# Performance work log

Measured on AMD Instinct MI355X. Metric: run time of the kernel, lower is better.

The kernel has to match this reference:

```python
import jax, jax.numpy as jnp
import numpy as np

B, T, F = 4096, 256, 20
VOCAB, EMB = 1281, 4
UNITS = (64, 32, 32, 32)


def setup_inputs() -> dict:
    key = jax.random.key(0)
    ks = jax.random.split(key, 16)
    feats = jax.random.normal(ks[0], (B, T, F), jnp.float32)
    ids = jax.random.randint(ks[1], (B, T), 0, VOCAB).astype(jnp.float32)
    input_tensor = feats.at[:, :, 1].set(ids)  # column 1 = org ids
    W_emb = jax.random.normal(ks[2], (VOCAB, EMB), jnp.float32) * 0.1
    in_dims = (F - 2 + 1 + EMB,) + UNITS[:-1]  # (23, 64, 32, 32)
    out = {"input_tensor": input_tensor, "W_emb": W_emb}
    for i, (din, u) in enumerate(zip(in_dims, UNITS)):
        out[f"k{i}"] = jax.random.normal(ks[3 + 3 * i], (din, 3 * u), jnp.float32) * 0.1
        out[f"rk{i}"] = jax.random.normal(ks[4 + 3 * i], (u, 3 * u), jnp.float32) * 0.1
        out[f"b{i}"] = jnp.zeros((2, 3 * u), jnp.float32)  # [input_bias, recurrent_bias] (reset_after)
    out["Wd"] = jax.random.normal(ks[15], (UNITS[-1], 2), jnp.float32) * 0.1
    out["bd"] = jnp.zeros((2,), jnp.float32)
    return out


def _gru(h, x, k, rk, b):
    # Keras GRUCell, reset_after=True (TF2 default)
    mx = x @ k + b[0]
    mh = h @ rk + b[1]
    xz, xr, xh = jnp.split(mx, 3, axis=-1)
    hz, hr, hh = jnp.split(mh, 3, axis=-1)
    z = jax.nn.sigmoid(xz + hz)
    r = jax.nn.sigmoid(xr + hr)
    hc = jnp.tanh(xh + r * hh)
    return z * h + (1.0 - z) * hc


def reference(input_tensor, W_emb, k0, rk0, b0, k1, rk1, b1, k2, rk2, b2, k3, rk3, b3, Wd, bd):
    f0 = input_tensor[:, :, :1]                      # [B,T,1]
    ids = input_tensor[:, :, 1].astype(jnp.int32)    # [B,T]
    rest = input_tensor[:, :, 2:]                    # [B,T,F-2]
    emb = W_emb[ids]                                 # [B,T,EMB]
    x = jnp.concatenate([f0, rest, emb], axis=-1)    # [B,T,F+3]
    xs = jnp.swapaxes(x, 0, 1)                       # [T,B,F+3]
    bsz = x.shape[0]
    h_init = tuple(jnp.zeros((bsz, u), x.dtype) for u in UNITS)
    layer_params = ((k0, rk0, b0), (k1, rk1, b1), (k2, rk2, b2), (k3, rk3, b3))

    def step(carry, xt):
        hs = []
        inp = xt
        for h, (k, rk, b) in zip(carry, layer_params):
            h = _gru(h, inp, k, rk, b)
            hs.append(h)
            inp = h
        return tuple(hs), None

    hs, _ = jax.lax.scan(step, h_init, xs)
    # return_sequences + [:, -1, :] == final hidden state of last layer
    logits = hs[-1] @ Wd + bd
    return jax.nn.softmax(logits, axis=-1)
```

## Files before the change

### kernel.cpp

```cpp
#include <hip/hip_runtime.h>


typedef __attribute__((ext_vector_type(8))) __bf16 bf16x8;
typedef __attribute__((ext_vector_type(4))) float f32x4;

#define TT 256
#define FF 20
#define BT 16
#define CH 64
#define SH0 72
#define SH1 40
#define XSTR 648
#define NTHR 768

__device__ __forceinline__ f32x4 mfma16(bf16x8 a, bf16x8 b, f32x4 c) {
  return __builtin_amdgcn_mfma_f32_16x16x32_bf16(a, b, c, 0, 0, 0);
}

__device__ __forceinline__ float sigm(float x) {
  return __builtin_amdgcn_rcpf(1.f + __builtin_amdgcn_exp2f(-1.44269504f * x));
}
__device__ __forceinline__ float tanh_(float x) {
  return __builtin_amdgcn_rcpf(1.f + __builtin_amdgcn_exp2f(-2.88539008f * x)) * 2.f - 1.f;
}

__device__ __forceinline__ bf16x8 bfragW(const float* W, int Kreal, int N,
                                         int ncol, int kbase) {
  bf16x8 r;
#pragma unroll
  for (int j = 0; j < 8; ++j) {
    int k = kbase + j;
    r[j] = (__bf16)(k < Kreal ? W[k * N + ncol] : 0.f);
  }
  return r;
}

extern "C" __global__ void __launch_bounds__(NTHR, 3)
gru4(const float* __restrict__ inp, const float* __restrict__ Wemb,
     const float* __restrict__ k0, const float* __restrict__ rk0, const float* __restrict__ b0,
     const float* __restrict__ k1, const float* __restrict__ rk1, const float* __restrict__ b1,
     const float* __restrict__ k2, const float* __restrict__ rk2, const float* __restrict__ b2,
     const float* __restrict__ k3, const float* __restrict__ rk3, const float* __restrict__ b3,
     const float* __restrict__ Wd, const float* __restrict__ bd,
     float* __restrict__ out)
{
  __shared__ __align__(16) __bf16 x_ch[CH * XSTR];
  __shared__ __align__(16) __bf16 h0_lds[2][BT * SH0];
  __shared__ __align__(16) __bf16 h1_lds[2][BT * SH1];
  __shared__ __align__(16) __bf16 h2_lds[2][BT * SH1];
  __shared__ __align__(16) __bf16 h3_lds[2][BT * SH1];
  __shared__ __align__(16) float h3f[BT * 32];

  const int tid  = threadIdx.x;
  const int lane = tid & 63;
  const int w    = tid >> 6;
  const int col  = lane & 15;
  const int kb   = (lane >> 4) * 8;
  const int rowq = (lane >> 4) * 4;
  const long bbase = (long)blockIdx.x * BT;
  const float* binp = inp + bbase * TT * FF;

  bf16x8 zf;
#pragma unroll
  for (int j = 0; j < 8; ++j) zf[j] = (__bf16)0.f;

  bf16x8 Wz0 = zf, Wz1 = zf, Wz2 = zf;
  bf16x8 Wr0 = zf, Wr1 = zf, Wr2 = zf;
  bf16x8 Wgx0 = zf, Wgx1 = zf, Wgx2 = zf;
  bf16x8 Wgh0 = zf, Wgh1 = zf, Wgh2 = zf;
  float bz = 0.f, br = 0.f, bxh = 0.f, bhh = 0.f;
  const __bf16 *A0b = x_ch, *A1b = x_ch, *A2b = x_ch;
  int D0 = 0, D1 = 0, D2 = 0;
  __bf16* Wwr0 = (__bf16*)h3f;
  int WD = 0, wstride = SH1;
  int lay = 0;
  bool doLo = false, doHi = false, threeA = false;

  if (w < 6) {
    lay = 0; threeA = true;
    const int sl = (w < 4) ? (w >> 1) : (w - 2);
    doLo = (w >= 4) || ((w & 1) == 0);
    doHi = (w >= 4) || ((w & 1) == 1);
    const int u = sl * 16 + col;
    Wz0 = bfragW(k0, 23, 192, u, kb);
    Wz1 = bfragW(rk0, 64, 192, u, kb);
    Wz2 = bfragW(rk0, 64, 192, u, 32 + kb);
    Wr0 = bfragW(k0, 23, 192, 64 + u, kb);
    Wr1 = bfragW(rk0, 64, 192, 64 + u, kb);
    Wr2 = bfragW(rk0, 64, 192, 64 + u, 32 + kb);
    Wgx0 = bfragW(k0, 23, 192, 128 + u, kb);
    Wgh1 = bfragW(rk0, 64, 192, 128 + u, kb);
    Wgh2 = bfragW(rk0, 64, 192, 128 + u, 32 + kb);
    bz  = b0[u] + b0[192 + u];
    br  = b0[64 + u] + b0[192 + 64 + u];
    bxh = b0[128 + u];
    bhh = b0[192 + 128 + u];
    A1b = &h0_lds[0][col * SH0 + kb];      D1 = BT * SH0;
    A2b = &h0_lds[0][col * SH0 + 32 + kb]; D2 = BT * SH0;
    Wwr0 = &h0_lds[0][rowq * SH0 + sl * 16 + col];
    WD = BT * SH0; wstride = SH0;
  } else if (w < 8) {
    lay = 1; threeA = true; doLo = doHi = true;
    const int u = (w - 6) * 16 + col;
    Wz0 = bfragW(k1, 64, 96, u, kb);
    Wz1 = bfragW(k1, 64, 96, u, 32 + kb);
    Wz2 = bfragW(rk1, 32, 96, u, kb);
    Wr0 = bfragW(k1, 64, 96, 32 + u, kb);
    Wr1 = bfragW(k1, 64, 96, 32 + u, 32 + kb);
    Wr2 = bfragW(rk1, 32, 96, 32 + u, kb);
    Wgx0 = bfragW(k1, 64, 96, 64 + u, kb);
    Wgx1 = bfragW(k1, 64, 96, 64 + u, 32 + kb);
    Wgh2 = bfragW(rk1, 32, 96, 64 + u, kb);
    bz  = b1[u] + b1[96 + u];
    br  = b1[32 + u] + b1[96 + 32 + u];
    bxh = b1[64 + u];
    bhh = b1[96 + 64 + u];
    A0b = &h0_lds[0][col * SH0 + kb];      D0 = BT * SH0;
    A1b = &h0_lds[0][col * SH0 + 32 + kb]; D1 = BT * SH0;
    A2b = &h1_lds[0][col * SH1 + kb];      D2 = BT * SH1;
    Wwr0 = &h1_lds[0][rowq * SH1 + (w - 6) * 16 + col];
    WD = BT * SH1; wstride = SH1;
  } else if (w < 10) {
    lay = 2; threeA = false; doLo = doHi = true;
    const int u = (w - 8) * 16 + col;
    Wz0 = bfragW(k2, 32, 96, u, kb);
    Wz1 = bfragW(rk2, 32, 96, u, kb);
    Wr0 = bfragW(k2, 32, 96, 32 + u, kb);
    Wr1 = bfragW(rk2, 32, 96, 32 + u, kb);
    Wgx0 = bfragW(k2, 32, 96, 64 + u, kb);
    Wgh1 = bfragW(rk2, 32, 96, 64 + u, kb);
    bz  = b2[u] + b2[96 + u];
    br  = b2[32 + u] + b2[96 + 32 + u];
    bxh = b2[64 + u];
    bhh = b2[96 + 64 + u];
    A0b = &h1_lds[0][col * SH1 + kb]; D0 = BT * SH1;
    A1b = &h2_lds[0][col * SH1 + kb]; D1 = BT * SH1;
    A2b = A1b; D2 = D1;
    Wwr0 = &h2_lds[0][rowq * SH1 + (w - 8) * 16 + col];
    WD = BT * SH1; wstride = SH1;
  } else {
    lay = 3; threeA = false; doLo = doHi = true;
    const int u = (w - 10) * 16 + col;
    Wz0 = bfragW(k3, 32, 96, u, kb);
    Wz1 = bfragW(rk3, 32, 96, u, kb);
    Wr0 = bfragW(k3, 32, 96, 32 + u, kb);
    Wr1 = bfragW(rk3, 32, 96, 32 + u, kb);
    Wgx0 = bfragW(k3, 32, 96, 64 + u, kb);
    Wgh1 = bfragW(rk3, 32, 96, 64 + u, kb);
    bz  = b3[u] + b3[96 + u];
    br  = b3[32 + u] + b3[96 + 32 + u];
    bxh = b3[64 + u];
    bhh = b3[96 + 64 + u];
    A0b = &h2_lds[0][col * SH1 + kb]; D0 = BT * SH1;
    A1b = &h3_lds[0][col * SH1 + kb]; D1 = BT * SH1;
    A2b = A1b; D2 = D1;
    Wwr0 = &h3_lds[0][rowq * SH1 + (w - 10) * 16 + col];
    WD = BT * SH1; wstride = SH1;
  }

  const __bf16* xb = &x_ch[col * 40 + kb];

  {
    __bf16* p0 = (__bf16*)h0_lds;
    for (int i = tid; i < 2 * BT * SH0; i += NTHR) p0[i] = (__bf16)0.f;
    __bf16* p1 = (__bf16*)h1_lds;
    __bf16* p2 = (__bf16*)h2_lds;
    __bf16* p3 = (__bf16*)h3_lds;
    for (int i = tid; i < 2 * BT * SH1; i += NTHR) {
      p1[i] = (__bf16)0.f; p2[i] = (__bf16)0.f; p3[i] = (__bf16)0.f;
    }
  }
  float hreg[4] = {0.f, 0.f, 0.f, 0.f};
  __syncthreads();

  for (int s = 0; s < TT + 3; ++s) {
    if ((s & (CH - 1)) == 0 && s < TT) {
      for (int idx = tid; idx < BT * CH; idx += NTHR) {
        const int row = idx >> 6;
        const int tg  = idx & (CH - 1);
        const float* p = binp + ((long)row * TT + s + tg) * FF;
        float4 v0 = *(const float4*)(p);
        float4 v1 = *(const float4*)(p + 4);
        float4 v2 = *(const float4*)(p + 8);
        float4 v3 = *(const float4*)(p + 12);
        float4 v4 = *(const float4*)(p + 16);
        float4 e  = *(const float4*)(Wemb + 4 * (int)v0.y);
        __bf16* d = &x_ch[tg * XSTR + row * 40];
        bf16x8 q0 = {(__bf16)v0.x, (__bf16)v0.z, (__bf16)v0.w, (__bf16)v1.x,
                     (__bf16)v1.y, (__bf16)v1.z, (__bf16)v1.w, (__bf16)v2.x};
        bf16x8 q1 = {(__bf16)v2.y, (__bf16)v2.z, (__bf16)v2.w, (__bf16)v3.x,
                     (__bf16)v3.y, (__bf16)v3.z, (__bf16)v3.w, (__bf16)v4.x};
        bf16x8 q2 = {(__bf16)v4.y, (__bf16)v4.z, (__bf16)v4.w, (__bf16)e.x,
                     (__bf16)e.y,  (__bf16)e.z,  (__bf16)e.w,  (__bf16)0.f};
        *(bf16x8*)(d)      = q0;
        *(bf16x8*)(d + 8)  = q1;
        *(bf16x8*)(d + 16) = q2;
        *(bf16x8*)(d + 24) = zf;
      }
      __syncthreads();
    }

    const int pb = (s + 1) & 1;
    const int qb = s & 1;
    const int t  = s - lay;

    if (t >= 0 && t < TT) {
      const __bf16* a0p = (lay == 0) ? (xb + (s & (CH - 1)) * XSTR)
                                     : (A0b + pb * D0);
      bf16x8 A0 = *(const bf16x8*)a0p;
      bf16x8 A1 = *(const bf16x8*)(A1b + pb * D1);
      f32x4 az  = {bz, bz, bz, bz};
      f32x4 ar  = {br, br, br, br};
      f32x4 axh = {bxh, bxh, bxh, bxh};
      f32x4 ahh = {bhh, bhh, bhh, bhh};
      az  = mfma16(A0, Wz0, az);   az  = mfma16(A1, Wz1, az);
      ar  = mfma16(A0, Wr0, ar);   ar  = mfma16(A1, Wr1, ar);
      axh = mfma16(A0, Wgx0, axh); axh = mfma16(A1, Wgx1, axh);
      ahh = mfma16(A0, Wgh0, ahh); ahh = mfma16(A1, Wgh1, ahh);
      if (threeA) {
        bf16x8 A2 = *(const bf16x8*)(A2b + pb * D2);
        az  = mfma16(A2, Wz2, az);
        ar  = mfma16(A2, Wr2, ar);
        axh = mfma16(A2, Wgx2, axh);
        ahh = mfma16(A2, Wgh2, ahh);
      }
      __bf16* wr = Wwr0 + qb * WD;

#define GATE(r) { \
        float z  = sigm(az[r]); \
        float rg = sigm(ar[r]); \
        float hc = tanh_(fmaf(rg, ahh[r], axh[r])); \
        float hn = fmaf(z, hreg[r] - hc, hc); \
        hreg[r] = hn; \
        wr[(r) * wstride] = (__bf16)hn; }

      if (doLo) { GATE(0); GATE(1); }
      if (doHi) { GATE(2); GATE(3); }
#undef GATE
    }

    __syncthreads();
  }

  if (w >= 10) {
#pragma unroll
    for (int r = 0; r < 4; ++r)
      h3f[(rowq + r) * 32 + (w - 10) * 16 + col] = hreg[r];
  }
  __syncthreads();

  if (tid < BT) {
    float l0 = bd[0], l1 = bd[1];
#pragma unroll
    for (int u = 0; u < 32; ++u) {
      float h = h3f[tid * 32 + u];
      l0 = fmaf(h, Wd[2 * u], l0);
      l1 = fmaf(h, Wd[2 * u + 1], l1);
    }
    float m = fmaxf(l0, l1);
    float e0 = __builtin_amdgcn_exp2f((l0 - m) * 1.44269504f);
    float e1 = __builtin_amdgcn_exp2f((l1 - m) * 1.44269504f);
    float inv = 1.f / (e0 + e1);
    out[(bbase + tid) * 2 + 0] = e0 * inv;
    out[(bbase + tid) * 2 + 1] = e1 * inv;
  }
}

extern "C" void kernel_launch(void* const* d_in, const int* in_sizes, int n_in,
                              void* d_out, int out_size, void* d_ws, size_t ws_size,
                              hipStream_t stream) {
  const float* inp  = (const float*)d_in[0];
  const float* Wemb = (const float*)d_in[1];
  const float* k0   = (const float*)d_in[2];
  const float* rk0  = (const float*)d_in[3];
  const float* b0   = (const float*)d_in[4];
  const float* k1   = (const float*)d_in[5];
  const float* rk1  = (const float*)d_in[6];
  const float* b1   = (const float*)d_in[7];
  const float* k2   = (const float*)d_in[8];
  const float* rk2  = (const float*)d_in[9];
  const float* b2   = (const float*)d_in[10];
  const float* k3   = (const float*)d_in[11];
  const float* rk3  = (const float*)d_in[12];
  const float* b3   = (const float*)d_in[13];
  const float* Wd   = (const float*)d_in[14];
  const float* bd   = (const float*)d_in[15];
  float* out = (float*)d_out;

  const int Btot = in_sizes[0] / (TT * FF);
  dim3 grid(Btot / BT);
  gru4<<<grid, NTHR, 0, stream>>>(inp, Wemb, k0, rk0, b0, k1, rk1, b1,
                                  k2, rk2, b2, k3, rk3, b3, Wd, bd, out);
}
```

Baseline: 345.5 us.

## Software-pipeline GRU steps so gate math precedes barrier and MFMAs follow

```diff
diff --git a/kernel.cpp b/kernel.cpp
--- a/kernel.cpp
+++ b/kernel.cpp
@@ -173,74 +173,82 @@
   float hreg[4] = {0.f, 0.f, 0.f, 0.f};
   __syncthreads();
 
-  for (int s = 0; s < TT + 3; ++s) {
-    if ((s & (CH - 1)) == 0 && s < TT) {
-      for (int idx = tid; idx < BT * CH; idx += NTHR) {
-        const int row = idx >> 6;
-        const int tg  = idx & (CH - 1);
-        const float* p = binp + ((long)row * TT + s + tg) * FF;
-        float4 v0 = *(const float4*)(p);
-        float4 v1 = *(const float4*)(p + 4);
-        float4 v2 = *(const float4*)(p + 8);
-        float4 v3 = *(const float4*)(p + 12);
-        float4 v4 = *(const float4*)(p + 16);
-        float4 e  = *(const float4*)(Wemb + 4 * (int)v0.y);
-        __bf16* d = &x_ch[tg * XSTR + row * 40];
-        bf16x8 q0 = {(__bf16)v0.x, (__bf16)v0.z, (__bf16)v0.w, (__bf16)v1.x,
-                     (__bf16)v1.y, (__bf16)v1.z, (__bf16)v1.w, (__bf16)v2.x};
-        bf16x8 q1 = {(__bf16)v2.y, (__bf16)v2.z, (__bf16)v2.w, (__bf16)v3.x,
-                     (__bf16)v3.y, (__bf16)v3.z, (__bf16)v3.w, (__bf16)v4.x};
-        bf16x8 q2 = {(__bf16)v4.y, (__bf16)v4.z, (__bf16)v4.w, (__bf16)e.x,
-                     (__bf16)e.y,  (__bf16)e.z,  (__bf16)e.w,  (__bf16)0.f};
-        *(bf16x8*)(d)      = q0;
-        *(bf16x8*)(d + 8)  = q1;
-        *(bf16x8*)(d + 16) = q2;
-        *(bf16x8*)(d + 24) = zf;
-      }
-      __syncthreads();
+  auto stageX = [&](int s) {
+    for (int idx = tid; idx < BT * CH; idx += NTHR) {
+      const int row = idx >> 6;
+      const int tq  = idx & (CH - 1);
+      const float* p = binp + ((long)row * TT + s + tq) * FF;
+      float4 v0 = *(const float4*)(p);
+      float4 v1 = *(const float4*)(p + 4);
+      float4 v2 = *(const float4*)(p + 8);
+      float4 v3 = *(const float4*)(p + 12);
+      float4 v4 = *(const float4*)(p + 16);
+      float4 e  = *(const float4*)(Wemb + 4 * (int)v0.y);
+      __bf16* d = &x_ch[tq * XSTR + row * 40];
+      bf16x8 q0 = {(__bf16)v0.x, (__bf16)v0.z, (__bf16)v0.w, (__bf16)v1.x,
+                   (__bf16)v1.y, (__bf16)v1.z, (__bf16)v1.w, (__bf16)v2.x};
+      bf16x8 q1 = {(__bf16)v2.y, (__bf16)v2.z, (__bf16)v2.w, (__bf16)v3.x,
+                   (__bf16)v3.y, (__bf16)v3.z, (__bf16)v3.w, (__bf16)v4.x};
+      bf16x8 q2 = {(__bf16)v4.y, (__bf16)v4.z, (__bf16)v4.w, (__bf16)e.x,
+                   (__bf16)e.y,  (__bf16)e.z,  (__bf16)e.w,  (__bf16)0.f};
+      *(bf16x8*)(d)      = q0;
+      *(bf16x8*)(d + 8)  = q1;
+      *(bf16x8*)(d + 16) = q2;
+      *(bf16x8*)(d + 24) = zf;
     }
-
-    const int pb = (s + 1) & 1;
-    const int qb = s & 1;
-    const int t  = s - lay;
-
-    if (t >= 0 && t < TT) {
-      const __bf16* a0p = (lay == 0) ? (xb + (s & (CH - 1)) * XSTR)
-                                     : (A0b + pb * D0);
-      bf16x8 A0 = *(const bf16x8*)a0p;
-      bf16x8 A1 = *(const bf16x8*)(A1b + pb * D1);
-      f32x4 az  = {bz, bz, bz, bz};
-      f32x4 ar  = {br, br, br, br};
-      f32x4 axh = {bxh, bxh, bxh, bxh};
-      f32x4 ahh = {bhh, bhh, bhh, bhh};
-      az  = mfma16(A0, Wz0, az);   az  = mfma16(A1, Wz1, az);
-      ar  = mfma16(A0, Wr0, ar);   ar  = mfma16(A1, Wr1, ar);
-      axh = mfma16(A0, Wgx0, axh); axh = mfma16(A1, Wgx1, axh);
-      ahh = mfma16(A0, Wgh0, ahh); ahh = mfma16(A1, Wgh1, ahh);
-      if (threeA) {
-        bf16x8 A2 = *(const bf16x8*)(A2b + pb * D2);
-        az  = mfma16(A2, Wz2, az);
-        ar  = mfma16(A2, Wr2, ar);
-        axh = mfma16(A2, Wgx2, axh);
-        ahh = mfma16(A2, Wgh2, ahh);
-      }
-      __bf16* wr = Wwr0 + qb * WD;
-
-#define GATE(r) { \
-        float z  = sigm(az[r]); \
-        float rg = sigm(ar[r]); \
-        float hc = tanh_(fmaf(rg, ahh[r], axh[r])); \
-        float hn = fmaf(z, hreg[r] - hc, hc); \
-        hreg[r] = hn; \
-        wr[(r) * wstride] = (__bf16)hn; }
-
-      if (doLo) { GATE(0); GATE(1); }
-      if (doHi) { GATE(2); GATE(3); }
+  };
+
+  f32x4 az0 = {0.f,0.f,0.f,0.f}, ar0 = az0, axh0 = az0, ahh0 = az0;
+  f32x4 az1 = az0, ar1 = az0, axh1 = az0, ahh1 = az0;
+
+#define GATE(O, r) { \
+    float z  = sigm(az##O[r]); \
+    float rg = sigm(ar##O[r]); \
+    float hc = tanh_(fmaf(rg, ahh##O[r], axh##O[r])); \
+    float hn = fmaf(z, hreg[r] - hc, hc); \
+    hreg[r] = hn; \
+    wr[(r) * wstride] = (__bf16)hn; }
+
+#define ITER(S, N, O) { \
+    const int tg_ = (S) - lay - 1; \
+    if (tg_ >= 0 && tg_ < TT) { \
+      __bf16* wr = Wwr0 + ((S) & 1) * WD; \
+      if (doLo) { GATE(O, 0) GATE(O, 1) } \
+      if (doHi) { GATE(O, 2) GATE(O, 3) } \
+    } \
+    __syncthreads(); \
+    if (((S) & (CH - 1)) == 0 && (S) < TT) { stageX(S); __syncthreads(); } \
+    const int tm_ = (S) - lay; \
+    if (tm_ >= 0 && tm_ < TT) { \
+      const int rb_ = (S) & 1; \
+      const __bf16* a0p = (lay == 0) ? (xb + ((S) & (CH - 1)) * XSTR) \
+                                     : (A0b + rb_ * D0); \
+      bf16x8 A0 = *(const bf16x8*)a0p; \
+      bf16x8 A1 = *(const bf16x8*)(A1b + rb_ * D1); \
+      az##N  = (f32x4){bz, bz, bz, bz}; \
+      ar##N  = (f32x4){br, br, br, br}; \
+      axh##N = (f32x4){bxh, bxh, bxh, bxh}; \
+      ahh##N = (f32x4){bhh, bhh, bhh, bhh}; \
+      az##N  = mfma16(A0, Wz0, az##N);   az##N  = mfma16(A1, Wz1, az##N); \
+      ar##N  = mfma16(A0, Wr0, ar##N);   ar##N  = mfma16(A1, Wr1, ar##N); \
+      axh##N = mfma16(A0, Wgx0, axh##N); axh##N = mfma16(A1, Wgx1, axh##N); \
+      ahh##N = mfma16(A0, Wgh0, ahh##N); ahh##N = mfma16(A1, Wgh1, ahh##N); \
+      if (threeA) { \
+        bf16x8 A2 = *(const bf16x8*)(A2b + rb_ * D2); \
+        az##N  = mfma16(A2, Wz2, az##N); \
+        ar##N  = mfma16(A2, Wr2, ar##N); \
+        axh##N = mfma16(A2, Wgx2, axh##N); \
+        ahh##N = mfma16(A2, Wgh2, ahh##N); \
+      } \
+    } \
+  }
+
+  for (int s2 = 0; s2 < TT + 4; s2 += 2) {
+    ITER(s2, 0, 1)
+    ITER(s2 + 1, 1, 0)
+  }
+#undef ITER
 #undef GATE
-    }
-
-    __syncthreads();
-  }
 
   if (w >= 10) {
 #pragma unroll
```

Result: no change. 347.3 us (+0.5%).

## Assign one wavefront per GRU layer and sync once per eight-step supergroup

Applied to the files above, without the earlier changes.

```diff
diff --git a/kernel.cpp b/kernel.cpp
--- a/kernel.cpp
+++ b/kernel.cpp
@@ -7,11 +7,16 @@
 #define TT 256
 #define FF 20
 #define BT 16
-#define CH 64
-#define SH0 72
-#define SH1 40
-#define XSTR 648
-#define NTHR 768
+#define KS 8
+#define NSUP 35
+#define XSTR 40
+#define H0STR 72
+#define H1STR 40
+#define XPL (16 * XSTR)
+#define H0PL (16 * H0STR)
+#define H1PL (16 * H1STR)
+#define W0PL (16 * H0STR)
+#define NTHR 256
 
 __device__ __forceinline__ f32x4 mfma16(bf16x8 a, bf16x8 b, f32x4 c) {
   return __builtin_amdgcn_mfma_f32_16x16x32_bf16(a, b, c, 0, 0, 0);
@@ -35,7 +40,7 @@
   return r;
 }
 
-extern "C" __global__ void __launch_bounds__(NTHR, 3)
+extern "C" __global__ void __launch_bounds__(NTHR, 1)
 gru4(const float* __restrict__ inp, const float* __restrict__ Wemb,
      const float* __restrict__ k0, const float* __restrict__ rk0, const float* __restrict__ b0,
      const float* __restrict__ k1, const float* __restrict__ rk1, const float* __restrict__ b1,
@@ -44,19 +49,20 @@
      const float* __restrict__ Wd, const float* __restrict__ bd,
      float* __restrict__ out)
 {
-  __shared__ __align__(16) __bf16 x_ch[CH * XSTR];
-  __shared__ __align__(16) __bf16 h0_lds[2][BT * SH0];
-  __shared__ __align__(16) __bf16 h1_lds[2][BT * SH1];
-  __shared__ __align__(16) __bf16 h2_lds[2][BT * SH1];
-  __shared__ __align__(16) __bf16 h3_lds[2][BT * SH1];
+  __shared__ __align__(16) __bf16 xring[16 * XPL];
+  __shared__ __align__(16) __bf16 h0ring[16 * H0PL];
+  __shared__ __align__(16) __bf16 h1ring[16 * H1PL];
+  __shared__ __align__(16) __bf16 h2ring[16 * H1PL];
+  __shared__ __align__(16) __bf16 h3s[2 * H1PL];
+  __shared__ __align__(16) __bf16 w0p[12 * W0PL];
   __shared__ __align__(16) float h3f[BT * 32];
 
   const int tid  = threadIdx.x;
   const int lane = tid & 63;
   const int w    = tid >> 6;
-  const int col  = lane & 15;
+  const int c    = lane & 15;
   const int kb   = (lane >> 4) * 8;
-  const int rowq = (lane >> 4) * 4;
+  const int rq   = (lane >> 4) * 4;
   const long bbase = (long)blockIdx.x * BT;
   const float* binp = inp + bbase * TT * FF;
 
@@ -64,191 +70,357 @@
 #pragma unroll
   for (int j = 0; j < 8; ++j) zf[j] = (__bf16)0.f;
 
-  bf16x8 Wz0 = zf, Wz1 = zf, Wz2 = zf;
-  bf16x8 Wr0 = zf, Wr1 = zf, Wr2 = zf;
-  bf16x8 Wgx0 = zf, Wgx1 = zf, Wgx2 = zf;
-  bf16x8 Wgh0 = zf, Wgh1 = zf, Wgh2 = zf;
-  float bz = 0.f, br = 0.f, bxh = 0.f, bhh = 0.f;
-  const __bf16 *A0b = x_ch, *A1b = x_ch, *A2b = x_ch;
-  int D0 = 0, D1 = 0, D2 = 0;
-  __bf16* Wwr0 = (__bf16*)h3f;
-  int WD = 0, wstride = SH1;
-  int lay = 0;
-  bool doLo = false, doHi = false, threeA = false;
-
-  if (w < 6) {
-    lay = 0; threeA = true;
-    const int sl = (w < 4) ? (w >> 1) : (w - 2);
-    doLo = (w >= 4) || ((w & 1) == 0);
-    doHi = (w >= 4) || ((w & 1) == 1);
-    const int u = sl * 16 + col;
-    Wz0 = bfragW(k0, 23, 192, u, kb);
-    Wz1 = bfragW(rk0, 64, 192, u, kb);
-    Wz2 = bfragW(rk0, 64, 192, u, 32 + kb);
-    Wr0 = bfragW(k0, 23, 192, 64 + u, kb);
-    Wr1 = bfragW(rk0, 64, 192, 64 + u, kb);
-    Wr2 = bfragW(rk0, 64, 192, 64 + u, 32 + kb);
-    Wgx0 = bfragW(k0, 23, 192, 128 + u, kb);
-    Wgh1 = bfragW(rk0, 64, 192, 128 + u, kb);
-    Wgh2 = bfragW(rk0, 64, 192, 128 + u, 32 + kb);
-    bz  = b0[u] + b0[192 + u];
-    br  = b0[64 + u] + b0[192 + 64 + u];
-    bxh = b0[128 + u];
-    bhh = b0[192 + 128 + u];
-    A1b = &h0_lds[0][col * SH0 + kb];      D1 = BT * SH0;
-    A2b = &h0_lds[0][col * SH0 + 32 + kb]; D2 = BT * SH0;
-    Wwr0 = &h0_lds[0][rowq * SH0 + sl * 16 + col];
-    WD = BT * SH0; wstride = SH0;
-  } else if (w < 8) {
-    lay = 1; threeA = true; doLo = doHi = true;
-    const int u = (w - 6) * 16 + col;
-    Wz0 = bfragW(k1, 64, 96, u, kb);
-    Wz1 = bfragW(k1, 64, 96, u, 32 + kb);
-    Wz2 = bfragW(rk1, 32, 96, u, kb);
-    Wr0 = bfragW(k1, 64, 96, 32 + u, kb);
-    Wr1 = bfragW(k1, 64, 96, 32 + u, 32 + kb);
-    Wr2 = bfragW(rk1, 32, 96, 32 + u, kb);
-    Wgx0 = bfragW(k1, 64, 96, 64 + u, kb);
-    Wgx1 = bfragW(k1, 64, 96, 64 + u, 32 + kb);
-    Wgh2 = bfragW(rk1, 32, 96, 64 + u, kb);
-    bz  = b1[u] + b1[96 + u];
-    br  = b1[32 + u] + b1[96 + 32 + u];
-    bxh = b1[64 + u];
-    bhh = b1[96 + 64 + u];
-    A0b = &h0_lds[0][col * SH0 + kb];      D0 = BT * SH0;
-    A1b = &h0_lds[0][col * SH0 + 32 + kb]; D1 = BT * SH0;
-    A2b = &h1_lds[0][col * SH1 + kb];      D2 = BT * SH1;
-    Wwr0 = &h1_lds[0][rowq * SH1 + (w - 6) * 16 + col];
-    WD = BT * SH1; wstride = SH1;
-  } else if (w < 10) {
-    lay = 2; threeA = false; doLo = doHi = true;
-    const int u = (w - 8) * 16 + col;
-    Wz0 = bfragW(k2, 32, 96, u, kb);
-    Wz1 = bfragW(rk2, 32, 96, u, kb);
-    Wr0 = bfragW(k2, 32, 96, 32 + u, kb);
-    Wr1 = bfragW(rk2, 32, 96, 32 + u, kb);
-    Wgx0 = bfragW(k2, 32, 96, 64 + u, kb);
-    Wgh1 = bfragW(rk2, 32, 96, 64 + u, kb);
-    bz  = b2[u] + b2[96 + u];
-    br  = b2[32 + u] + b2[96 + 32 + u];
-    bxh = b2[64 + u];
-    bhh = b2[96 + 64 + u];
-    A0b = &h1_lds[0][col * SH1 + kb]; D0 = BT * SH1;
-    A1b = &h2_lds[0][col * SH1 + kb]; D1 = BT * SH1;
-    A2b = A1b; D2 = D1;
-    Wwr0 = &h2_lds[0][rowq * SH1 + (w - 8) * 16 + col];
-    WD = BT * SH1; wstride = SH1;
+  for (int i = tid; i < 16 * H0PL; i += NTHR) h0ring[i] = (__bf16)0.f;
+  for (int i = tid; i < 16 * H1PL; i += NTHR) { h1ring[i] = (__bf16)0.f; h2ring[i] = (__bf16)0.f; }
+  for (int i = tid; i < 2 * H1PL; i += NTHR) h3s[i] = (__bf16)0.f;
+  for (int e = tid; e < 12 * 16 * 64; e += NTHR) {
+    int p = e >> 10, rem = e & 1023, cc = rem >> 6, kk = rem & 63;
+    int g = p >> 2;
+    int gb = (g == 0) ? 0 : (g == 1) ? 64 : 128;
+    w0p[p * W0PL + cc * H0STR + kk] = (__bf16)rk0[kk * 192 + gb + (p & 3) * 16 + cc];
+  }
+
+  auto stageX = [&](int tstart) {
+    int j = tid - 128;
+    if (j >= 0) {
+      int tp = j >> 4, row = j & 15;
+      int t = tstart + tp;
+      const float* p = binp + ((long)row * TT + t) * FF;
+      float4 v0 = *(const float4*)(p);
+      float4 v1 = *(const float4*)(p + 4);
+      float4 v2 = *(const float4*)(p + 8);
+      float4 v3 = *(const float4*)(p + 12);
+      float4 v4 = *(const float4*)(p + 16);
+      float4 e  = *(const float4*)(Wemb + 4 * (int)v0.y);
+      __bf16* d = &xring[(t & 15) * XPL + row * XSTR];
+      bf16x8 q0 = {(__bf16)v0.x, (__bf16)v0.z, (__bf16)v0.w, (__bf16)v1.x,
+                   (__bf16)v1.y, (__bf16)v1.z, (__bf16)v1.w, (__bf16)v2.x};
+      bf16x8 q1 = {(__bf16)v2.y, (__bf16)v2.z, (__bf16)v2.w, (__bf16)v3.x,
+                   (__bf16)v3.y, (__bf16)v3.z, (__bf16)v3.w, (__bf16)v4.x};
+      bf16x8 q2 = {(__bf16)v4.y, (__bf16)v4.z, (__bf16)v4.w, (__bf16)e.x,
+                   (__bf16)e.y,  (__bf16)e.z,  (__bf16)e.w,  (__bf16)0.f};
+      *(bf16x8*)(d)      = q0;
+      *(bf16x8*)(d + 8)  = q1;
+      *(bf16x8*)(d + 16) = q2;
+      *(bf16x8*)(d + 24) = zf;
+    }
+  };
+  stageX(0);
+  __syncthreads();
+
+  if (w == 0) {
+    bf16x8 WzX[4], WrX[4], WxX[4];
+    f32x4 bZ[4], bR[4], bXH[4], bHH[4];
+#pragma unroll
+    for (int sl = 0; sl < 4; ++sl) {
+      const int u = sl * 16 + c;
+      WzX[sl] = bfragW(k0, 23, 192, u, kb);
+      WrX[sl] = bfragW(k0, 23, 192, 64 + u, kb);
+      WxX[sl] = bfragW(k0, 23, 192, 128 + u, kb);
+      float vz = b0[u] + b0[192 + u];
+      float vr = b0[64 + u] + b0[192 + 64 + u];
+      float vx = b0[128 + u];
+      float vh = b0[192 + 128 + u];
+      bZ[sl]  = (f32x4){vz, vz, vz, vz};
+      bR[sl]  = (f32x4){vr, vr, vr, vr};
+      bXH[sl] = (f32x4){vx, vx, vx, vx};
+      bHH[sl] = (f32x4){vh, vh, vh, vh};
+    }
+    f32x4 az[4], ar[4], ax[4], ah[4];
+    float hp[4][4];
+#pragma unroll
+    for (int sl = 0; sl < 4; ++sl)
+#pragma unroll
+      for (int r = 0; r < 4; ++r) hp[sl][r] = 0.f;
+
+    auto mfmaS = [&](int t) {
+      bf16x8 Ax = *(const bf16x8*)&xring[(t & 15) * XPL + c * XSTR + kb];
+#pragma unroll
+      for (int sl = 0; sl < 4; ++sl) {
+        az[sl] = mfma16(Ax, WzX[sl], bZ[sl]);
+        ar[sl] = mfma16(Ax, WrX[sl], bR[sl]);
+        ax[sl] = mfma16(Ax, WxX[sl], bXH[sl]);
+      }
+      const __bf16* hb = &h0ring[((t - 1) & 15) * H0PL + c * H0STR];
+      bf16x8 Ah1 = *(const bf16x8*)&hb[kb];
+      bf16x8 Ah2 = *(const bf16x8*)&hb[32 + kb];
+      const __bf16* wp = &w0p[c * H0STR + kb];
+#pragma unroll
+      for (int sl = 0; sl < 4; ++sl) {
+        bf16x8 f1 = *(const bf16x8*)&wp[sl * W0PL];
+        bf16x8 f2 = *(const bf16x8*)&wp[sl * W0PL + 32];
+        az[sl] = mfma16(Ah1, f1, az[sl]);
+        az[sl] = mfma16(Ah2, f2, az[sl]);
+      }
+#pragma unroll
+      for (int sl = 0; sl < 4; ++sl) {
+        bf16x8 f1 = *(const bf16x8*)&wp[(4 + sl) * W0PL];
+        bf16x8 f2 = *(const bf16x8*)&wp[(4 + sl) * W0PL + 32];
+        ar[sl] = mfma16(Ah1, f1, ar[sl]);
+        ar[sl] = mfma16(Ah2, f2, ar[sl]);
+      }
+#pragma unroll
+      for (int sl = 0; sl < 4; ++sl) {
+        bf16x8 f1 = *(const bf16x8*)&wp[(8 + sl) * W0PL];
+        bf16x8 f2 = *(const bf16x8*)&wp[(8 + sl) * W0PL + 32];
+        ah[sl] = mfma16(Ah1, f1, bHH[sl]);
+        ah[sl] = mfma16(Ah2, f2, ah[sl]);
+      }
+    };
+    auto gateS = [&](int t) {
+      __bf16* wr = &h0ring[(t & 15) * H0PL + rq * H0STR];
+#pragma unroll
+      for (int sl = 0; sl < 4; ++sl)
+#pragma unroll
+        for (int r = 0; r < 4; ++r) {
+          float z  = sigm(az[sl][r]);
+          float rg = sigm(ar[sl][r]);
+          float hc = tanh_(fmaf(rg, ah[sl][r], ax[sl][r]));
+          float hn = fmaf(z, hp[sl][r] - hc, hc);
+          hp[sl][r] = hn;
+          wr[r * H0STR + sl * 16 + c] = (__bf16)hn;
+        }
+    };
+
+    for (int sg = 0; sg < NSUP; ++sg) {
+      const int tb = sg * KS;
+      if (tb < TT) {
+        mfmaS(tb);
+#pragma unroll 1
+        for (int k2 = 0; k2 < KS - 1; ++k2) {
+          gateS(tb + k2);
+          mfmaS(tb + k2 + 1);
+        }
+        gateS(tb + KS - 1);
+      }
+      __syncthreads();
+    }
+  } else if (w == 1) {
+    bf16x8 Wz1[2], Wz2[2], WzH[2], Wr1[2], Wr2[2], WrH[2], Wx1[2], Wx2[2], WhH[2];
+    f32x4 bZ[2], bR[2], bXH[2], bHH[2];
+#pragma unroll
+    for (int t2 = 0; t2 < 2; ++t2) {
+      const int u = t2 * 16 + c;
+      Wz1[t2] = bfragW(k1, 64, 96, u, kb);
+      Wz2[t2] = bfragW(k1, 64, 96, u, 32 + kb);
+      WzH[t2] = bfragW(rk1, 32, 96, u, kb);
+      Wr1[t2] = bfragW(k1, 64, 96, 32 + u, kb);
+      Wr2[t2] = bfragW(k1, 64, 96, 32 + u, 32 + kb);
+      WrH[t2] = bfragW(rk1, 32, 96, 32 + u, kb);
+      Wx1[t2] = bfragW(k1, 64, 96, 64 + u, kb);
+      Wx2[t2] = bfragW(k1, 64, 96, 64 + u, 32 + kb);
+      WhH[t2] = bfragW(rk1, 32, 96, 64 + u, kb);
+      float vz = b1[u] + b1[96 + u];
+      float vr = b1[32 + u] + b1[96 + 32 + u];
+      float vx = b1[64 + u];
+      float vh = b1[96 + 64 + u];
+      bZ[t2]  = (f32x4){vz, vz, vz, vz};
+      bR[t2]  = (f32x4){vr, vr, vr, vr};
+      bXH[t2] = (f32x4){vx, vx, vx, vx};
+      bHH[t2] = (f32x4){vh, vh, vh, vh};
+    }
+    f32x4 az[2], ar[2], ax[2], ah[2];
+    float hp[2][4];
+#pragma unroll
+    for (int t2 = 0; t2 < 2; ++t2)
+#pragma unroll
+      for (int r = 0; r < 4; ++r) hp[t2][r] = 0.f;
+
+    auto mfmaS = [&](int t) {
+      const __bf16* xb = &h0ring[(t & 15) * H0PL + c * H0STR];
+      bf16x8 Ax1 = *(const bf16x8*)&xb[kb];
+      bf16x8 Ax2 = *(const bf16x8*)&xb[32 + kb];
+      bf16x8 Ah  = *(const bf16x8*)&h1ring[((t - 1) & 15) * H1PL + c * H1STR + kb];
+#pragma unroll
+      for (int t2 = 0; t2 < 2; ++t2) {
+        az[t2] = mfma16(Ax1, Wz1[t2], bZ[t2]);
+        az[t2] = mfma16(Ax2, Wz2[t2], az[t2]);
+        az[t2] = mfma16(Ah,  WzH[t2], az[t2]);
+        ar[t2] = mfma16(Ax1, Wr1[t2], bR[t2]);
+        ar[t2] = mfma16(Ax2, Wr2[t2], ar[t2]);
+        ar[t2] = mfma16(Ah,  WrH[t2], ar[t2]);
+        ax[t2] = mfma16(Ax1, Wx1[t2], bXH[t2]);
+        ax[t2] = mfma16(Ax2, Wx2[t2], ax[t2]);
+        ah[t2] = mfma16(Ah,  WhH[t2], bHH[t2]);
+      }
+    };
+    auto gateS = [&](int t) {
+      __bf16* wr = &h1ring[(t & 15) * H1PL + rq * H1STR];
+#pragma unroll
+      for (int t2 = 0; t2 < 2; ++t2)
+#pragma unroll
+        for (int r = 0; r < 4; ++r) {
+          float z  = sigm(az[t2][r]);
+          float rg = sigm(ar[t2][r]);
+          float hc = tanh_(fmaf(rg, ah[t2][r], ax[t2][r]));
+          float hn = fmaf(z, hp[t2][r] - hc, hc);
+          hp[t2][r] = hn;
+          wr[r * H1STR + t2 * 16 + c] = (__bf16)hn;
+        }
+    };
+
+    for (int sg = 0; sg < NSUP; ++sg) {
+      const int tb = (sg - 1) * KS;
+      if (tb >= 0 && tb < TT) {
+        mfmaS(tb);
+#pragma unroll 1
+        for (int k2 = 0; k2 < KS - 1; ++k2) {
+          gateS(tb + k2);
+          mfmaS(tb + k2 + 1);
+        }
+        gateS(tb + KS - 1);
+      }
+      __syncthreads();
+    }
+  } else if (w == 2) {
+    bf16x8 WzX[2], WzH[2], WrX[2], WrH[2], WxX[2], WhH[2];
+    f32x4 bZ[2], bR[2], bXH[2], bHH[2];
+#pragma unroll
+    for (int t2 = 0; t2 < 2; ++t2) {
+      const int u = t2 * 16 + c;
+      WzX[t2] = bfragW(k2, 32, 96, u, kb);
+      WzH[t2] = bfragW(rk2, 32, 96, u, kb);
+      WrX[t2] = bfragW(k2, 32, 96, 32 + u, kb);
+      WrH[t2] = bfragW(rk2, 32, 96, 32 + u, kb);
+      WxX[t2] = bfragW(k2, 32, 96, 64 + u, kb);
+      WhH[t2] = bfragW(rk2, 32, 96, 64 + u, kb);
+      float vz = b2[u] + b2[96 + u];
+      float vr = b2[32 + u] + b2[96 + 32 + u];
+      float vx = b2[64 + u];
+      float vh = b2[96 + 64 + u];
+      bZ[t2]  = (f32x4){vz, vz, vz, vz};
+      bR[t2]  = (f32x4){vr, vr, vr, vr};
+      bXH[t2] = (f32x4){vx, vx, vx, vx};
+      bHH[t2] = (f32x4){vh, vh, vh, vh};
+    }
+    f32x4 az[2], ar[2], ax[2], ah[2];
+    float hp[2][4];
+#pragma unroll
+    for (int t2 = 0; t2 < 2; ++t2)
+#pragma unroll
+      for (int r = 0; r < 4; ++r) hp[t2][r] = 0.f;
+
+    auto mfmaS = [&](int t) {
+      bf16x8 Ax = *(const bf16x8*)&h1ring[(t & 15) * H1PL + c * H1STR + kb];
+      bf16x8 Ah = *(const bf16x8*)&h2ring[((t - 1) & 15) * H1PL + c * H1STR + kb];
+#pragma unroll
+      for (int t2 = 0; t2 < 2; ++t2) {
+        az[t2] = mfma16(Ax, WzX[t2], bZ[t2]);
+        az[t2] = mfma16(Ah, WzH[t2], az[t2]);
+        ar[t2] = mfma16(Ax, WrX[t2], bR[t2]);
+        ar[t2] = mfma16(Ah, WrH[t2], ar[t2]);
+        ax[t2] = mfma16(Ax, WxX[t2], bXH[t2]);
+        ah[t2] = mfma16(Ah, WhH[t2], bHH[t2]);
+      }
+    };
+    auto gateS = [&](int t) {
+      __bf16* wr = &h2ring[(t & 15) * H1PL + rq * H1STR];
+#pragma unroll
+      for (int t2 = 0; t2 < 2; ++t2)
+#pragma unroll
+        for (int r = 0; r < 4; ++r) {
+          float z  = sigm(az[t2][r]);
+          float rg = sigm(ar[t2][r]);
+          float hc = tanh_(fmaf(rg, ah[t2][r], ax[t2][r]));
+          float hn = fmaf(z, hp[t2][r] - hc, hc);
+          hp[t2][r] = hn;
+          wr[r * H1STR + t2 * 16 + c] = (__bf16)hn;
+        }
+    };
+
+    for (int sg = 0; sg < NSUP; ++sg) {
+      const int tb = (sg - 2) * KS;
+      if (tb >= 0 && tb < TT) {
+        mfmaS(tb);
+#pragma unroll 1
+        for (int k2 = 0; k2 < KS - 1; ++k2) {
+          gateS(tb + k2);
+          mfmaS(tb + k2 + 1);
+        }
+        gateS(tb + KS - 1);
+      }
+      if (sg < 31) stageX((sg + 1) * KS);
+      __syncthreads();
+    }
   } else {
-    lay = 3; threeA = false; doLo = doHi = true;
-    const int u = (w - 10) * 16 + col;
-    Wz0 = bfragW(k3, 32, 96, u, kb);
-    Wz1 = bfragW(rk3, 32, 96, u, kb);
-    Wr0 = bfragW(k3, 32, 96, 32 + u, kb);
-    Wr1 = bfragW(rk3, 32, 96, 32 + u, kb);
-    Wgx0 = bfragW(k3, 32, 96, 64 + u, kb);
-    Wgh1 = bfragW(rk3, 32, 96, 64 + u, kb);
-    bz  = b3[u] + b3[96 + u];
-    br  = b3[32 + u] + b3[96 + 32 + u];
-    bxh = b3[64 + u];
-    bhh = b3[96 + 64 + u];
-    A0b = &h2_lds[0][col * SH1 + kb]; D0 = BT * SH1;
-    A1b = &h3_lds[0][col * SH1 + kb]; D1 = BT * SH1;
-    A2b = A1b; D2 = D1;
-    Wwr0 = &h3_lds[0][rowq * SH1 + (w - 10) * 16 + col];
-    WD = BT * SH1; wstride = SH1;
+    bf16x8 WzX[2], WzH[2], WrX[2], WrH[2], WxX[2], WhH[2];
+    f32x4 bZ[2], bR[2], bXH[2], bHH[2];
+#pragma unroll
+    for (int t2 = 0; t2 < 2; ++t2) {
+      const int u = t2 * 16 + c;
+      WzX[t2] = bfragW(k3, 32, 96, u, kb);
+      WzH[t2] = bfragW(rk3, 32, 96, u, kb);
+      WrX[t2] = bfragW(k3, 32, 96, 32 + u, kb);
+      WrH[t2] = bfragW(rk3, 32, 96, 32 + u, kb);
+      WxX[t2] = bfragW(k3, 32, 96, 64 + u, kb);
+      WhH[t2] = bfragW(rk3, 32, 96, 64 + u, kb);
+      float vz = b3[u] + b3[96 + u];
+      float vr = b3[32 + u] + b3[96 + 32 + u];
+      float vx = b3[64 + u];
+      float vh = b3[96 + 64 + u];
+      bZ[t2]  = (f32x4){vz, vz, vz, vz};
+      bR[t2]  = (f32x4){vr, vr, vr, vr};
+      bXH[t2] = (f32x4){vx, vx, vx, vx};
+      bHH[t2] = (f32x4){vh, vh, vh, vh};
+    }
+    f32x4 az[2], ar[2], ax[2], ah[2];
+    float hp[2][4];
+#pragma unroll
+    for (int t2 = 0; t2 < 2; ++t2)
+#pragma unroll
+      for (int r = 0; r < 4; ++r) hp[t2][r] = 0.f;
+
+    auto mfmaS = [&](int t) {
+      bf16x8 Ax = *(const bf16x8*)&h2ring[(t & 15) * H1PL + c * H1STR + kb];
+      bf16x8 Ah = *(const bf16x8*)&h3s[((t - 1) & 1) * H1PL + c * H1STR + kb];
+#pragma unroll
+      for (int t2 = 0; t2 < 2; ++t2) {
+        az[t2] = mfma16(Ax, WzX[t2], bZ[t2]);
+        az[t2] = mfma16(Ah, WzH[t2], az[t2]);
+        ar[t2] = mfma16(Ax, WrX[t2], bR[t2]);
+        ar[t2] = mfma16(Ah, WrH[t2], ar[t2]);
+        ax[t2] = mfma16(Ax, WxX[t2], bXH[t2]);
+        ah[t2] = mfma16(Ah, WhH[t2], bHH[t2]);
+      }
+    };
+    auto gateS = [&](int t) {
+      __bf16* wr = &h3s[(t & 1) * H1PL + rq * H1STR];
+#pragma unroll
+      for (int t2 = 0; t2 < 2; ++t2)
+#pragma unroll
+        for (int r = 0; r < 4; ++r) {
+          float z  = sigm(az[t2][r]);
+          float rg = sigm(ar[t2][r]);
+          float hc = tanh_(fmaf(rg, ah[t2][r], ax[t2][r]));
+          float hn = fmaf(z, hp[t2][r] - hc, hc);
+          hp[t2][r] = hn;
+          wr[r * H1STR + t2 * 16 + c] = (__bf16)hn;
+        }
+    };
+
+    for (int sg = 0; sg < NSUP; ++sg) {
+      const int tb = (sg - 3) * KS;
+      if (tb >= 0 && tb < TT) {
+        mfmaS(tb);
+#pragma unroll 1
+        for (int k2 = 0; k2 < KS - 1; ++k2) {
+          gateS(tb + k2);
+          mfmaS(tb + k2 + 1);
+        }
+        gateS(tb + KS - 1);
+      }
+      if (sg < 31) stageX((sg + 1) * KS);
+      __syncthreads();
+    }
+
+#pragma unroll
+    for (int t2 = 0; t2 < 2; ++t2)
+#pragma unroll
+      for (int r = 0; r < 4; ++r)
+        h3f[(rq + r) * 32 + t2 * 16 + c] = hp[t2][r];
   }
 
-  const __bf16* xb = &x_ch[col * 40 + kb];
-
-  {
-    __bf16* p0 = (__bf16*)h0_lds;
-    for (int i = tid; i < 2 * BT * SH0; i += NTHR) p0[i] = (__bf16)0.f;
-    __bf16* p1 = (__bf16*)h1_lds;
-    __bf16* p2 = (__bf16*)h2_lds;
-    __bf16* p3 = (__bf16*)h3_lds;
-    for (int i = tid; i < 2 * BT * SH1; i += NTHR) {
-      p1[i] = (__bf16)0.f; p2[i] = (__bf16)0.f; p3[i] = (__bf16)0.f;
-    }
-  }
-  float hreg[4] = {0.f, 0.f, 0.f, 0.f};
   __syncthreads();
-
-  for (int s = 0; s < TT + 3; ++s) {
-    if ((s & (CH - 1)) == 0 && s < TT) {
-      for (int idx = tid; idx < BT * CH; idx += NTHR) {
-        const int row = idx >> 6;
-        const int tg  = idx & (CH - 1);
-        const float* p = binp + ((long)row * TT + s + tg) * FF;
-        float4 v0 = *(const float4*)(p);
-        float4 v1 = *(const float4*)(p + 4);
-        float4 v2 = *(const float4*)(p + 8);
-        float4 v3 = *(const float4*)(p + 12);
-        float4 v4 = *(const float4*)(p + 16);
-        float4 e  = *(const float4*)(Wemb + 4 * (int)v0.y);
-        __bf16* d = &x_ch[tg * XSTR + row * 40];
-        bf16x8 q0 = {(__bf16)v0.x, (__bf16)v0.z, (__bf16)v0.w, (__bf16)v1.x,
-                     (__bf16)v1.y, (__bf16)v1.z, (__bf16)v1.w, (__bf16)v2.x};
-        bf16x8 q1 = {(__bf16)v2.y, (__bf16)v2.z, (__bf16)v2.w, (__bf16)v3.x,
-                     (__bf16)v3.y, (__bf16)v3.z, (__bf16)v3.w, (__bf16)v4.x};
-        bf16x8 q2 = {(__bf16)v4.y, (__bf16)v4.z, (__bf16)v4.w, (__bf16)e.x,
-                     (__bf16)e.y,  (__bf16)e.z,  (__bf16)e.w,  (__bf16)0.f};
-        *(bf16x8*)(d)      = q0;
-        *(bf16x8*)(d + 8)  = q1;
-        *(bf16x8*)(d + 16) = q2;
-        *(bf16x8*)(d + 24) = zf;
-      }
-      __syncthreads();
-    }
-
-    const int pb = (s + 1) & 1;
-    const int qb = s & 1;
-    const int t  = s - lay;
-
-    if (t >= 0 && t < TT) {
-      const __bf16* a0p = (lay == 0) ? (xb + (s & (CH - 1)) * XSTR)
-                                     : (A0b + pb * D0);
-      bf16x8 A0 = *(const bf16x8*)a0p;
-      bf16x8 A1 = *(const bf16x8*)(A1b + pb * D1);
-      f32x4 az  = {bz, bz, bz, bz};
-      f32x4 ar  = {br, br, br, br};
-      f32x4 axh = {bxh, bxh, bxh, bxh};
-      f32x4 ahh = {bhh, bhh, bhh, bhh};
-      az  = mfma16(A0, Wz0, az);   az  = mfma16(A1, Wz1, az);
-      ar  = mfma16(A0, Wr0, ar);   ar  = mfma16(A1, Wr1, ar);
-      axh = mfma16(A0, Wgx0, axh); axh = mfma16(A1, Wgx1, axh);
-      ahh = mfma16(A0, Wgh0, ahh); ahh = mfma16(A1, Wgh1, ahh);
-      if (threeA) {
-        bf16x8 A2 = *(const bf16x8*)(A2b + pb * D2);
-        az  = mfma16(A2, Wz2, az);
-        ar  = mfma16(A2, Wr2, ar);
-        axh = mfma16(A2, Wgx2, axh);
-        ahh = mfma16(A2, Wgh2, ahh);
-      }
-      __bf16* wr = Wwr0 + qb * WD;
-
-#define GATE(r) { \
-        float z  = sigm(az[r]); \
-        float rg = sigm(ar[r]); \
-        float hc = tanh_(fmaf(rg, ahh[r], axh[r])); \
-        float hn = fmaf(z, hreg[r] - hc, hc); \
-        hreg[r] = hn; \
-        wr[(r) * wstride] = (__bf16)hn; }
-
-      if (doLo) { GATE(0); GATE(1); }
-      if (doHi) { GATE(2); GATE(3); }
-#undef GATE
-    }
-
-    __syncthreads();
-  }
-
-  if (w >= 10) {
-#pragma unroll
-    for (int r = 0; r < 4; ++r)
-      h3f[(rowq + r) * 32 + (w - 10) * 16 + col] = hreg[r];
-  }
-  __syncthreads();
-
   if (tid < BT) {
     float l0 = bd[0], l1 = bd[1];
 #pragma unroll
```

New measurement: 445.6 us. 1.29x slower.

## Replace per-step block barriers with LDS counter-based producer/consumer sync

Applied to the files above, without the earlier changes.

```diff
diff --git a/kernel.cpp b/kernel.cpp
--- a/kernel.cpp
+++ b/kernel.cpp
@@ -34,6 +34,15 @@
   }
   return r;
 }
+
+#define POLL(cptr, tgt) { \
+    while (*(volatile int*)(cptr) < (tgt)) {} \
+    __builtin_amdgcn_sched_barrier(0); \
+    asm volatile("" ::: "memory"); }
+
+#define SIGNAL(cptr) { \
+    asm volatile("s_waitcnt lgkmcnt(0)" ::: "memory"); \
+    if (lane == 0) atomicAdd((int*)(cptr), 1); }
 
 extern "C" __global__ void __launch_bounds__(NTHR, 3)
 gru4(const float* __restrict__ inp, const float* __restrict__ Wemb,
@@ -50,6 +59,7 @@
   __shared__ __align__(16) __bf16 h2_lds[2][BT * SH1];
   __shared__ __align__(16) __bf16 h3_lds[2][BT * SH1];
   __shared__ __align__(16) float h3f[BT * 32];
+  __shared__ int cnts[8];
 
   const int tid  = threadIdx.x;
   const int lane = tid & 63;
@@ -75,6 +85,10 @@
   int WD = 0, wstride = SH1;
   int lay = 0;
   bool doLo = false, doHi = false, threeA = false;
+  int* gBelow = (int*)&cnts[0]; int nBelow = 0;
+  int* gOwn   = (int*)&cnts[0]; int nOwn   = 0;
+  int* mOwn   = (int*)&cnts[4];
+  int* mAbove = (int*)&cnts[4]; int nAbove = 0;
 
   if (w < 6) {
     lay = 0; threeA = true;
@@ -99,6 +113,9 @@
     A2b = &h0_lds[0][col * SH0 + 32 + kb]; D2 = BT * SH0;
     Wwr0 = &h0_lds[0][rowq * SH0 + sl * 16 + col];
     WD = BT * SH0; wstride = SH0;
+    gOwn = (int*)&cnts[0]; nOwn = 6;
+    mOwn = (int*)&cnts[4];
+    mAbove = (int*)&cnts[5]; nAbove = 2;
   } else if (w < 8) {
     lay = 1; threeA = true; doLo = doHi = true;
     const int u = (w - 6) * 16 + col;
@@ -120,6 +137,10 @@
     A2b = &h1_lds[0][col * SH1 + kb];      D2 = BT * SH1;
     Wwr0 = &h1_lds[0][rowq * SH1 + (w - 6) * 16 + col];
     WD = BT * SH1; wstride = SH1;
+    gBelow = (int*)&cnts[0]; nBelow = 6;
+    gOwn = (int*)&cnts[1]; nOwn = 2;
+    mOwn = (int*)&cnts[5];
+    mAbove = (int*)&cnts[6]; nAbove = 2;
   } else if (w < 10) {
     lay = 2; threeA = false; doLo = doHi = true;
     const int u = (w - 8) * 16 + col;
@@ -138,6 +159,10 @@
     A2b = A1b; D2 = D1;
     Wwr0 = &h2_lds[0][rowq * SH1 + (w - 8) * 16 + col];
     WD = BT * SH1; wstride = SH1;
+    gBelow = (int*)&cnts[1]; nBelow = 2;
+    gOwn = (int*)&cnts[2]; nOwn = 2;
+    mOwn = (int*)&cnts[6];
+    mAbove = (int*)&cnts[7]; nAbove = 2;
   } else {
     lay = 3; threeA = false; doLo = doHi = true;
     const int u = (w - 10) * 16 + col;
@@ -156,7 +181,15 @@
     A2b = A1b; D2 = D1;
     Wwr0 = &h3_lds[0][rowq * SH1 + (w - 10) * 16 + col];
     WD = BT * SH1; wstride = SH1;
-  }
+    gBelow = (int*)&cnts[2]; nBelow = 2;
+    gOwn = (int*)&cnts[3]; nOwn = 2;
+    mOwn = (int*)&cnts[7];
+  }
+
+  const f32x4 BZ  = {bz, bz, bz, bz};
+  const f32x4 BR  = {br, br, br, br};
+  const f32x4 BXH = {bxh, bxh, bxh, bxh};
+  const f32x4 BHH = {bhh, bhh, bhh, bhh};
 
   const __bf16* xb = &x_ch[col * 40 + kb];
 
@@ -169,34 +202,48 @@
     for (int i = tid; i < 2 * BT * SH1; i += NTHR) {
       p1[i] = (__bf16)0.f; p2[i] = (__bf16)0.f; p3[i] = (__bf16)0.f;
     }
+    if (tid < 8) cnts[tid] = 0;
   }
   float hreg[4] = {0.f, 0.f, 0.f, 0.f};
   __syncthreads();
 
+  auto stageX = [&](int s) {
+    for (int idx = tid; idx < BT * CH; idx += NTHR) {
+      const int row = idx >> 6;
+      const int tg  = idx & (CH - 1);
+      const float* p = binp + ((long)row * TT + s + tg) * FF;
+      float4 v0 = *(const float4*)(p);
+      float4 v1 = *(const float4*)(p + 4);
+      float4 v2 = *(const float4*)(p + 8);
+      float4 v3 = *(const float4*)(p + 12);
+      float4 v4 = *(const float4*)(p + 16);
+      float4 e  = *(const float4*)(Wemb + 4 * (int)v0.y);
+      __bf16* d = &x_ch[tg * XSTR + row * 40];
+      bf16x8 q0 = {(__bf16)v0.x, (__bf16)v0.z, (__bf16)v0.w, (__bf16)v1.x,
+                   (__bf16)v1.y, (__bf16)v1.z, (__bf16)v1.w, (__bf16)v2.x};
+      bf16x8 q1 = {(__bf16)v2.y, (__bf16)v2.z, (__bf16)v2.w, (__bf16)v3.x,
+                   (__bf16)v3.y, (__bf16)v3.z, (__bf16)v3.w, (__bf16)v4.x};
+      bf16x8 q2 = {(__bf16)v4.y, (__bf16)v4.z, (__bf16)v4.w, (__bf16)e.x,
+                   (__bf16)e.y,  (__bf16)e.z,  (__bf16)e.w,  (__bf16)0.f};
+      *(bf16x8*)(d)      = q0;
+      *(bf16x8*)(d + 8)  = q1;
+      *(bf16x8*)(d + 16) = q2;
+      *(bf16x8*)(d + 24) = zf;
+    }
+  };
+
+#define GATE(r) { \
+    float z  = sigm(az[r]); \
+    float rg = sigm(ar[r]); \
+    float hc = tanh_(fmaf(rg, ahh[r], axh[r])); \
+    float hn = fmaf(z, hreg[r] - hc, hc); \
+    hreg[r] = hn; \
+    wr[(r) * wstride] = (__bf16)hn; }
+
   for (int s = 0; s < TT + 3; ++s) {
     if ((s & (CH - 1)) == 0 && s < TT) {
-      for (int idx = tid; idx < BT * CH; idx += NTHR) {
-        const int row = idx >> 6;
-        const int tg  = idx & (CH - 1);
-        const float* p = binp + ((long)row * TT + s + tg) * FF;
-        float4 v0 = *(const float4*)(p);
-        float4 v1 = *(const float4*)(p + 4);
-        float4 v2 = *(const float4*)(p + 8);
-        float4 v3 = *(const float4*)(p + 12);
-        float4 v4 = *(const float4*)(p + 16);
-        float4 e  = *(const float4*)(Wemb + 4 * (int)v0.y);
-        __bf16* d = &x_ch[tg * XSTR + row * 40];
-        bf16x8 q0 = {(__bf16)v0.x, (__bf16)v0.z, (__bf16)v0.w, (__bf16)v1.x,
-                     (__bf16)v1.y, (__bf16)v1.z, (__bf16)v1.w, (__bf16)v2.x};
-        bf16x8 q1 = {(__bf16)v2.y, (__bf16)v2.z, (__bf16)v2.w, (__bf16)v3.x,
-                     (__bf16)v3.y, (__bf16)v3.z, (__bf16)v3.w, (__bf16)v4.x};
-        bf16x8 q2 = {(__bf16)v4.y, (__bf16)v4.z, (__bf16)v4.w, (__bf16)e.x,
-                     (__bf16)e.y,  (__bf16)e.z,  (__bf16)e.w,  (__bf16)0.f};
-        *(bf16x8*)(d)      = q0;
-        *(bf16x8*)(d + 8)  = q1;
-        *(bf16x8*)(d + 16) = q2;
-        *(bf16x8*)(d + 24) = zf;
-      }
+      __syncthreads();
+      stageX(s);
       __syncthreads();
     }
 
@@ -205,18 +252,21 @@
     const int t  = s - lay;
 
     if (t >= 0 && t < TT) {
+      if (lay > 0) POLL(gBelow, nBelow * (t + 1));
       const __bf16* a0p = (lay == 0) ? (xb + (s & (CH - 1)) * XSTR)
                                      : (A0b + pb * D0);
       bf16x8 A0 = *(const bf16x8*)a0p;
+      f32x4 az  = mfma16(A0, Wz0, BZ);
+      f32x4 ar  = mfma16(A0, Wr0, BR);
+      f32x4 axh = mfma16(A0, Wgx0, BXH);
+      f32x4 ahh = mfma16(A0, Wgh0, BHH);
+
+      POLL(gOwn, nOwn * t);
       bf16x8 A1 = *(const bf16x8*)(A1b + pb * D1);
-      f32x4 az  = {bz, bz, bz, bz};
-      f32x4 ar  = {br, br, br, br};
-      f32x4 axh = {bxh, bxh, bxh, bxh};
-      f32x4 ahh = {bhh, bhh, bhh, bhh};
-      az  = mfma16(A0, Wz0, az);   az  = mfma16(A1, Wz1, az);
-      ar  = mfma16(A0, Wr0, ar);   ar  = mfma16(A1, Wr1, ar);
-      axh = mfma16(A0, Wgx0, axh); axh = mfma16(A1, Wgx1, axh);
-      ahh = mfma16(A0, Wgh0, ahh); ahh = mfma16(A1, Wgh1, ahh);
+      az  = mfma16(A1, Wz1, az);
+      ar  = mfma16(A1, Wr1, ar);
+      axh = mfma16(A1, Wgx1, axh);
+      ahh = mfma16(A1, Wgh1, ahh);
       if (threeA) {
         bf16x8 A2 = *(const bf16x8*)(A2b + pb * D2);
         az  = mfma16(A2, Wz2, az);
@@ -224,24 +274,19 @@
         axh = mfma16(A2, Wgx2, axh);
         ahh = mfma16(A2, Wgh2, ahh);
       }
+      SIGNAL(mOwn);
+
+      POLL(mOwn, nOwn * t);
+      if (lay < 3) POLL(mAbove, nAbove * (t - 1));
       __bf16* wr = Wwr0 + qb * WD;
-
-#define GATE(r) { \
-        float z  = sigm(az[r]); \
-        float rg = sigm(ar[r]); \
-        float hc = tanh_(fmaf(rg, ahh[r], axh[r])); \
-        float hn = fmaf(z, hreg[r] - hc, hc); \
-        hreg[r] = hn; \
-        wr[(r) * wstride] = (__bf16)hn; }
-
       if (doLo) { GATE(0); GATE(1); }
       if (doHi) { GATE(2); GATE(3); }
+      SIGNAL(gOwn);
+    }
+  }
 #undef GATE
-    }
-
-    __syncthreads();
-  }
-
+
+  __syncthreads();
   if (w >= 10) {
 #pragma unroll
     for (int r = 0; r < 4; ++r)
```

After: 373.7 us. +8.2%, slower.
